# Performance work log

Measured on AMD Instinct MI355X. Metric: run time of the kernel, lower is better.

## Reference

```python
import jax, jax.numpy as jnp
import numpy as np

RES = 7          # pooler_resolution
SR = 2           # sampling_ratio
SCALES = (1.0 / 8.0, 1.0 / 16.0, 1.0 / 32.0)
IMG = 1024.0


def roi_align_one(feat, boxes, scale):
    """torchvision roi_align (aligned=True) for one image.
    feat: [C,H,W]; boxes: [N,4] (x1,y1,x2,y2) -> [N,C,RES,RES]."""
    C, H, W = feat.shape
    N = boxes.shape[0]
    b = boxes * scale - 0.5  # aligned=True offset
    x1, y1, x2, y2 = b[:, 0], b[:, 1], b[:, 2], b[:, 3]
    bh = (y2 - y1) / RES
    bw = (x2 - x1) / RES
    # sample points within each bin: y = y1 + bh*(iy + (jy+0.5)/SR)
    grid = (jnp.arange(RES, dtype=feat.dtype)[:, None]
            + (jnp.arange(SR, dtype=feat.dtype)[None, :] + 0.5) / SR).reshape(-1)  # [RES*SR]
    ys = y1[:, None] + bh[:, None] * grid[None, :]  # [N, RES*SR]
    xs = x1[:, None] + bw[:, None] * grid[None, :]

    def prep(c, size):
        m = ((c >= -1.0) & (c <= size)).astype(feat.dtype)
        cc = jnp.clip(c, 0.0, size - 1)
        lo = jnp.minimum(jnp.floor(cc).astype(jnp.int32), size - 1)
        hi = jnp.minimum(lo + 1, size - 1)
        frac = cc - lo.astype(feat.dtype)
        return lo, hi, frac, m

    y0, y1i, ly, my = prep(ys, H)
    x0, x1i, lx, mx = prep(xs, W)
    hy, hx = 1.0 - ly, 1.0 - lx
    # gather 4 corners: result [C, N, Sy, Sx]
    f00 = feat[:, y0[:, :, None], x0[:, None, :]]
    f01 = feat[:, y0[:, :, None], x1i[:, None, :]]
    f10 = feat[:, y1i[:, :, None], x0[:, None, :]]
    f11 = feat[:, y1i[:, :, None], x1i[:, None, :]]
    val = (hy[:, :, None] * (hx[:, None, :] * f00 + lx[:, None, :] * f01)
           + ly[:, :, None] * (hx[:, None, :] * f10 + lx[:, None, :] * f11))
    val = val * (my[:, :, None] * mx[:, None, :])
    pooled = val.reshape(C, N, RES, SR, RES, SR).mean(axis=(3, 5))  # avg over samples per bin
    return pooled.transpose(1, 0, 2, 3)  # [N, C, RES, RES]


def setup_inputs() -> dict:
    key = jax.random.key(0)
    ks = jax.random.split(key, 12)
    B, N, C = 4, 512, 256
    feat_p3 = jax.random.normal(ks[0], (B, C, 128, 128), jnp.float32)
    feat_p4 = jax.random.normal(ks[1], (B, C, 64, 64), jnp.float32)
    feat_p5 = jax.random.normal(ks[2], (B, C, 32, 32), jnp.float32)
    # valid boxes inside a 1024x1024 image
    cx = jax.random.uniform(ks[3], (B, N), minval=0.0, maxval=IMG)
    cy = jax.random.uniform(ks[4], (B, N), minval=0.0, maxval=IMG)
    bw = jax.random.uniform(ks[5], (B, N), minval=16.0, maxval=256.0)
    bh = jax.random.uniform(ks[6], (B, N), minval=16.0, maxval=256.0)
    x1 = jnp.clip(cx - bw / 2, 0.0, IMG - 1.0)
    y1 = jnp.clip(cy - bh / 2, 0.0, IMG - 1.0)
    x2 = jnp.clip(cx + bw / 2, x1 + 1.0, IMG)
    y2 = jnp.clip(cy + bh / 2, y1 + 1.0, IMG)
    bbox2d = jnp.stack([x1, y1, x2, y2], axis=-1)  # [B,N,4]
    anchor_id = jax.random.randint(ks[7], (B, N, 1), 0, 9, dtype=jnp.int32)
    FLAT = C * RES * RES  # 12544
    FC = 1024
    OUT = 93
    W1 = jax.random.normal(ks[8], (FC, FLAT), jnp.float32) * 0.01
    b1 = jnp.zeros((FC,), jnp.float32)
    W2 = jax.random.normal(ks[9], (FC, FC), jnp.float32) * 0.02
    b2 = jnp.zeros((FC,), jnp.float32)
    Wp = jax.random.normal(ks[10], (OUT, FC), jnp.float32) * 0.02
    bp = jnp.zeros((OUT,), jnp.float32)
    return {"feat_p3": feat_p3, "feat_p4": feat_p4, "feat_p5": feat_p5,
            "bbox2d": bbox2d, "anchor_id": anchor_id,
            "W1": W1, "b1": b1, "W2": W2, "b2": b2, "Wp": Wp, "bp": bp}


def reference(feat_p3, feat_p4, feat_p5, bbox2d, anchor_id, W1, b1, W2, b2, Wp, bp):
    B, N = bbox2d.shape[:2]
    level = anchor_id[..., 0] // 3  # [B,N] in {0,1,2}
    feats = (feat_p3, feat_p4, feat_p5)
    # pool every proposal at every level, then pick its assigned level
    pooled = None
    for l, (scale, feat) in enumerate(zip(SCALES, feats)):
        p = jax.vmap(lambda f, bx, s=scale: roi_align_one(f, bx, s))(feat, bbox2d)  # [B,N,C,R,R]
        sel = (level == l).astype(p.dtype)[..., None, None, None]
        pooled = p * sel if pooled is None else pooled + p * sel
    x = pooled.reshape(B * N, -1)  # flatten [B*N, C*R*R]
    x = jax.nn.relu(x @ W1.T + b1)
    x = jax.nn.relu(x @ W2.T + b2)
    out = x @ Wp.T + bp
    return out.reshape(B, N, -1)  # [4, 512, 93]
```

## Files before the change

### kernel.cpp

```cpp
#include <hip/hip_runtime.h>
#include <hip/hip_bf16.h>

typedef unsigned short u16;
typedef __attribute__((ext_vector_type(8))) short short8;
typedef __attribute__((ext_vector_type(4))) float f32x4;
typedef __attribute__((ext_vector_type(4))) unsigned short us4;

__device__ __forceinline__ u16 f32_bf16(float f) {
  union { float f; unsigned int u; } v; v.f = f;
  unsigned int r = v.u + 0x7fffu + ((v.u >> 16) & 1u);
  return (u16)(r >> 16);
}
__device__ __forceinline__ float bf16_f32(u16 h) {
  union { unsigned int u; float f; } v; v.u = ((unsigned int)h) << 16; return v.f;
}

__device__ __forceinline__ void load_lds16(const void* g, void* l) {
  __builtin_amdgcn_global_load_lds((const __attribute__((address_space(1))) unsigned int*)g,
                                   (__attribute__((address_space(3))) unsigned int*)l,
                                   16, 0, 0);
}

__global__ __launch_bounds__(256) void cvt_f32_bf16(
    const float* __restrict__ src, u16* __restrict__ dst, int n4) {
  int i = blockIdx.x * 256 + threadIdx.x;
  if (i >= n4) return;
  const float4 v = ((const float4*)src)[i];
  unsigned long long pk = (unsigned long long)f32_bf16(v.x)
                        | ((unsigned long long)f32_bf16(v.y) << 16)
                        | ((unsigned long long)f32_bf16(v.z) << 32)
                        | ((unsigned long long)f32_bf16(v.w) << 48);
  ((unsigned long long*)dst)[i] = pk;
}

__global__ __launch_bounds__(256) void cvt_wp(
    const float* __restrict__ src, u16* __restrict__ dst) {
  int i = blockIdx.x * 256 + threadIdx.x;
  if (i >= 24576) return;
  int e = i * 4;
  float4 v = (e < 95232) ? ((const float4*)src)[i] : float4{0.f, 0.f, 0.f, 0.f};
  unsigned long long pk = (unsigned long long)f32_bf16(v.x)
                        | ((unsigned long long)f32_bf16(v.y) << 16)
                        | ((unsigned long long)f32_bf16(v.z) << 32)
                        | ((unsigned long long)f32_bf16(v.w) << 48);
  ((unsigned long long*)dst)[i] = pk;
}

__global__ __launch_bounds__(256) void transpose_feats(
    const float* __restrict__ p3, const float* __restrict__ p4, const float* __restrict__ p5,
    u16* __restrict__ t3, u16* __restrict__ t4, u16* __restrict__ t5) {
  const int bid = blockIdx.x;
  const float* src; u16* dst; int S, tile;
  if (bid < 16384)      { src = p3; dst = t3; S = 128; tile = bid; }
  else if (bid < 20480) { src = p4; dst = t4; S = 64;  tile = bid - 16384; }
  else                  { src = p5; dst = t5; S = 32;  tile = bid - 20480; }
  const int cchunk = tile & 3;
  const int fp0 = (tile >> 2) * 16;
  const int SS = S * S;
  const int b = fp0 / SS;
  const int pimg = fp0 - b * SS;
  __shared__ __align__(16) u16 lds[16 * 72];
  const int t = threadIdx.x;
  {
    const int cl = t >> 2, xv = t & 3;
    const int c = cchunk * 64 + cl;
    const float4 v = *(const float4*)(src + (size_t)(b * 256 + c) * SS + pimg + xv * 4);
    lds[(xv * 4 + 0) * 72 + cl] = f32_bf16(v.x);
    lds[(xv * 4 + 1) * 72 + cl] = f32_bf16(v.y);
    lds[(xv * 4 + 2) * 72 + cl] = f32_bf16(v.z);
    lds[(xv * 4 + 3) * 72 + cl] = f32_bf16(v.w);
  }
  __syncthreads();
  {
    const int xl = t >> 4, cg = (t & 15) * 4;
    const us4 h = *(const us4*)&lds[xl * 72 + cg];
    *(us4*)(dst + (size_t)(fp0 + xl) * 256 + cchunk * 64 + cg) = h;
  }
}

__global__ __launch_bounds__(256) void roi_pool2(
    const u16* __restrict__ t3, const u16* __restrict__ t4, const u16* __restrict__ t5,
    const float* __restrict__ bbox, const int* __restrict__ anchor,
    u16* __restrict__ X) {
  const int m = blockIdx.x;
  const int b = m >> 9;
  const int lvl = anchor[m] / 3;
  const u16* ft; int S; float scale;
  if (lvl == 0)      { ft = t3; S = 128; scale = 0.125f;   }
  else if (lvl == 1) { ft = t4; S = 64;  scale = 0.0625f;  }
  else               { ft = t5; S = 32;  scale = 0.03125f; }
  ft += (size_t)b * S * S * 256;
  const float* bx = bbox + (size_t)m * 4;
  const float x1 = bx[0] * scale - 0.5f;
  const float y1 = bx[1] * scale - 0.5f;
  const float bw = (bx[2] * scale - 0.5f - x1) * (1.0f / 7.0f);
  const float bh = (bx[3] * scale - 0.5f - y1) * (1.0f / 7.0f);
  const float fS = (float)S;

  __shared__ __align__(16) u16 xs[12544];
  const int wave = threadIdx.x >> 6, lane = threadIdx.x & 63;
  const int cbase = lane * 4;

  for (int p = wave; p < 49; p += 4) {
    const int py = p / 7, px = p - py * 7;
    float s0 = 0.f, s1 = 0.f, s2 = 0.f, s3 = 0.f;
#pragma unroll
    for (int sy = 0; sy < 2; ++sy) {
      const float y = y1 + bh * ((float)py + (sy ? 0.75f : 0.25f));
      const float my = (y >= -1.0f && y <= fS) ? 1.0f : 0.0f;
      const float cy = fminf(fmaxf(y, 0.0f), fS - 1.0f);
      const int y0 = (int)cy;
      const float ly = cy - (float)y0;
      const float hy = 1.0f - ly;
      const int y1i = (y0 + 1 < S) ? y0 + 1 : S - 1;
#pragma unroll
      for (int sx = 0; sx < 2; ++sx) {
        const float x = x1 + bw * ((float)px + (sx ? 0.75f : 0.25f));
        const float mx = (x >= -1.0f && x <= fS) ? 1.0f : 0.0f;
        const float cx = fminf(fmaxf(x, 0.0f), fS - 1.0f);
        const int x0 = (int)cx;
        const float lx = cx - (float)x0;
        const float hx = 1.0f - lx;
        const int x1i = (x0 + 1 < S) ? x0 + 1 : S - 1;
        const us4 f00 = *(const us4*)(ft + (size_t)(y0  * S + x0 ) * 256 + cbase);
        const us4 f01 = *(const us4*)(ft + (size_t)(y0  * S + x1i) * 256 + cbase);
        const us4 f10 = *(const us4*)(ft + (size_t)(y1i * S + x0 ) * 256 + cbase);
        const us4 f11 = *(const us4*)(ft + (size_t)(y1i * S + x1i) * 256 + cbase);
        const float msk = my * mx;
        const float w00 = hy * hx * msk, w01 = hy * lx * msk;
        const float w10 = ly * hx * msk, w11 = ly * lx * msk;
        s0 += w00 * bf16_f32(f00.x) + w01 * bf16_f32(f01.x) + w10 * bf16_f32(f10.x) + w11 * bf16_f32(f11.x);
        s1 += w00 * bf16_f32(f00.y) + w01 * bf16_f32(f01.y) + w10 * bf16_f32(f10.y) + w11 * bf16_f32(f11.y);
        s2 += w00 * bf16_f32(f00.z) + w01 * bf16_f32(f01.z) + w10 * bf16_f32(f10.z) + w11 * bf16_f32(f11.z);
        s3 += w00 * bf16_f32(f00.w) + w01 * bf16_f32(f01.w) + w10 * bf16_f32(f10.w) + w11 * bf16_f32(f11.w);
      }
    }
    xs[(cbase + 0) * 49 + p] = f32_bf16(s0 * 0.25f);
    xs[(cbase + 1) * 49 + p] = f32_bf16(s1 * 0.25f);
    xs[(cbase + 2) * 49 + p] = f32_bf16(s2 * 0.25f);
    xs[(cbase + 3) * 49 + p] = f32_bf16(s3 * 0.25f);
  }
  __syncthreads();
  uint4* dst = (uint4*)(X + (size_t)m * 12544);
  const uint4* srcl = (const uint4*)xs;
  for (int i = threadIdx.x; i < 1568; i += 256) dst[i] = srcl[i];
}

template<int NT>
__global__ __launch_bounds__(512, 2)
void gemm8_bt(const u16* __restrict__ A, int lda,
              const u16* __restrict__ B, int ldb,
              u16* __restrict__ Cpart, int M, int N,
              int mb, int nb) {
  __shared__ __align__(16) char lds[131072];
  const int tid = threadIdx.x;
  const int wave = tid >> 6, lane = tid & 63;
  const int wr = wave >> 2, wc = wave & 3;

  const int G = gridDim.x;
  const int bid = blockIdx.x;
  const int swz = (bid & 7) * (G >> 3) + (bid >> 3);
  const int x = swz % mb;
  const int rest = swz / mb;
  const int y = rest % nb;
  const int z = rest / nb;
  const int m0 = x * 256, n0 = y * 256;
  const int kb0 = z * (NT * 64);

  const int sb = ((lane & 7) ^ (lane >> 3)) << 4;
  const int rowb2 = 2 * (wave * 8 + (lane >> 3)) + (sb >> 6);
  const int keloff = (sb & 63) >> 1;

  const int frow = lane & 15;
  const int rh = frow >> 1;
  const int swb = ((((frow & 1) << 6) | ((lane >> 4) << 4))) ^ (rh << 4);
  const int a_rd = wr * 8192 + rh * 128 + swb;
  const int b_rd = wc * 4096 + rh * 128 + swb;

  f32x4 acc[8][4];
#pragma unroll
  for (int i = 0; i < 8; ++i)
#pragma unroll
    for (int j = 0; j < 4; ++j)
      acc[i][j] = f32x4{0.f, 0.f, 0.f, 0.f};

  auto stageAB = [&](int tile, int ph) {
    const int dst = ((tile & 1) * 2 + ph) * 16384;
    const int kel = kb0 + tile * 64 + ph * 32 + keloff;
#pragma unroll
    for (int i = 0; i < 2; ++i) {
      const u16* srcA = A + (size_t)(m0 + i * 128 + rowb2) * lda + kel;
      load_lds16(srcA, lds + dst + i * 8192 + wave * 1024);
    }
#pragma unroll
    for (int i = 0; i < 2; ++i) {
      const u16* srcB = B + (size_t)(n0 + i * 128 + rowb2) * ldb + kel;
      load_lds16(srcB, lds + 65536 + dst + i * 8192 + wave * 1024);
    }
  };

#define GPHASE(T, PH, VW, DOSTAGE)                                              \
  {                                                                             \
    asm volatile("s_waitcnt vmcnt(" VW ")" ::: "memory");                       \
    __builtin_amdgcn_s_barrier();                                               \
    __builtin_amdgcn_sched_barrier(0);                                          \
    const int hb_ = (((T) & 1) * 2 + (PH)) * 16384;                             \
    short8 af[8], bf[4];                                                        \
    _Pragma("unroll")                                                           \
    for (int fi = 0; fi < 8; ++fi)                                              \
      af[fi] = *(const short8*)(lds + hb_ + a_rd + fi * 1024);                  \
    _Pragma("unroll")                                                           \
    for (int fj = 0; fj < 4; ++fj)                                              \
      bf[fj] = *(const short8*)(lds + 65536 + hb_ + b_rd + fj * 1024);          \
    if (DOSTAGE) stageAB((T) + 1, (PH));                                        \
    __builtin_amdgcn_s_setprio(1);                                              \
    _Pragma("unroll")                                                           \
    for (int fi = 0; fi < 8; ++fi) {                                            \
      _Pragma("unroll")                                                         \
      for (int fj = 0; fj < 4; ++fj)                                            \
        acc[fi][fj] = __builtin_amdgcn_mfma_f32_16x16x32_bf16(af[fi], bf[fj],   \
                                                              acc[fi][fj], 0, 0, 0); \
    }                                                                           \
    __builtin_amdgcn_s_setprio(0);                                              \
  }

  stageAB(0, 0);
  stageAB(0, 1);
#pragma unroll 1
  for (int t = 0; t < NT - 1; ++t) {
    GPHASE(t, 0, "4", true);
    GPHASE(t, 1, "4", true);
  }
  GPHASE(NT - 1, 0, "4", false);
  GPHASE(NT - 1, 1, "0", false);
#undef GPHASE

  u16* Cp = Cpart + (size_t)z * ((size_t)M * N);
  const int rq = (lane >> 4) * 4;
  const int cq = lane & 15;
#pragma unroll
  for (int fi = 0; fi < 8; ++fi)
#pragma unroll
    for (int fj = 0; fj < 4; ++fj) {
      const int row = m0 + wr * 128 + fi * 16 + rq;
      const int col = n0 + wc * 64 + fj * 16 + cq;
#pragma unroll
      for (int q = 0; q < 4; ++q)
        Cp[(size_t)(row + q) * N + col] = f32_bf16(acc[fi][fj][q]);
    }
}

__global__ __launch_bounds__(256) void reduce_bias7(
    const u16* __restrict__ P7, const float* __restrict__ bias,
    u16* __restrict__ out) {
  const int i4 = (blockIdx.x * 256 + threadIdx.x) * 4;
  if (i4 >= 2097152) return;
  const int nb = i4 & 1023;
  float s0 = bias[nb], s1 = bias[nb + 1], s2 = bias[nb + 2], s3 = bias[nb + 3];
#pragma unroll
  for (int j = 0; j < 7; ++j) {
    const us4 v = *(const us4*)(P7 + (size_t)j * 2097152 + i4);
    s0 += bf16_f32(v.x); s1 += bf16_f32(v.y); s2 += bf16_f32(v.z); s3 += bf16_f32(v.w);
  }
  us4 o;
  o.x = f32_bf16(fmaxf(s0, 0.f)); o.y = f32_bf16(fmaxf(s1, 0.f));
  o.z = f32_bf16(fmaxf(s2, 0.f)); o.w = f32_bf16(fmaxf(s3, 0.f));
  *(us4*)(out + i4) = o;
}

template<int BM, int BN, int WGM, int WGN>
__global__ __launch_bounds__(256)
void gemm_bt_splitk(const u16* __restrict__ A, int lda,
                    const u16* __restrict__ B, int ldb,
                    float* __restrict__ Cpart, int M, int N, int Ksplit) {
  constexpr int BK = 64;
  constexpr int WM = BM / WGM, WN = BN / WGN;
  constexpr int FM = WM / 16, FN = WN / 16;
  constexpr int AITER = BM * BK / 2048;
  constexpr int BITER = BN * BK / 2048;
  __shared__ u16 Asm_[BM * BK];
  __shared__ u16 Bsm_[BN * BK];
  const int tid = threadIdx.x;
  const int wave = tid >> 6, lane = tid & 63;
  const int wr = wave / WGN, wc = wave % WGN;
  const int m0 = blockIdx.x * BM, n0 = blockIdx.y * BN;
  const int kbase0 = blockIdx.z * Ksplit;

  f32x4 acc[FM][FN];
#pragma unroll
  for (int i = 0; i < FM; ++i)
#pragma unroll
    for (int j = 0; j < FN; ++j)
      acc[i][j] = f32x4{0.0f, 0.0f, 0.0f, 0.0f};

  const int ar = tid >> 3;
  const int acsub = (tid & 7) * 8;
  const int fr = lane & 15;
  const int kq = (lane >> 4) * 8;

  for (int kt = 0; kt < Ksplit; kt += BK) {
    const int kb = kbase0 + kt;
#pragma unroll
    for (int it = 0; it < AITER; ++it) {
      const u16* src = A + (size_t)(m0 + it * 32 + ar) * lda + kb + acsub;
      load_lds16(src, (char*)Asm_ + it * 4096 + wave * 1024);
    }
#pragma unroll
    for (int it = 0; it < BITER; ++it) {
      const u16* src = B + (size_t)(n0 + it * 32 + ar) * ldb + kb + acsub;
      load_lds16(src, (char*)Bsm_ + it * 4096 + wave * 1024);
    }
    __syncthreads();
#pragma unroll
    for (int kk = 0; kk < BK; kk += 32) {
      short8 af[FM], bfr[FN];
#pragma unroll
      for (int i = 0; i < FM; ++i)
        af[i] = *(const short8*)(Asm_ + (wr * WM + i * 16 + fr) * BK + kk + kq);
#pragma unroll
      for (int j = 0; j < FN; ++j)
        bfr[j] = *(const short8*)(Bsm_ + (wc * WN + j * 16 + fr) * BK + kk + kq);
#pragma unroll
      for (int i = 0; i < FM; ++i)
#pragma unroll
        for (int j = 0; j < FN; ++j)
          acc[i][j] = __builtin_amdgcn_mfma_f32_16x16x32_bf16(af[i], bfr[j], acc[i][j], 0, 0, 0);
    }
    __syncthreads();
  }

  float* Cp = Cpart + (size_t)blockIdx.z * ((size_t)M * N);
  const int rq = (lane >> 4) * 4;
  const int cq = lane & 15;
#pragma unroll
  for (int i = 0; i < FM; ++i)
#pragma unroll
    for (int j = 0; j < FN; ++j) {
      const int row = m0 + wr * WM + i * 16 + rq;
      const int col = n0 + wc * WN + j * 16 + cq;
      float* o = Cp + (size_t)row * N + col;
#pragma unroll
      for (int q = 0; q < 4; ++q)
        o[(size_t)q * N] = acc[i][j][q];
    }
}

template<int S, bool RELU>
__global__ __launch_bounds__(256) void reduce_bias_bf16(
    const float* __restrict__ P, const float* __restrict__ bias,
    u16* __restrict__ out, int MN, int Nmask) {
  const int i = blockIdx.x * 256 + threadIdx.x;
  if (i >= MN) return;
  float s = bias[i & Nmask];
#pragma unroll
  for (int j = 0; j < S; ++j) s += P[(size_t)j * MN + i];
  if (RELU) s = fmaxf(s, 0.0f);
  out[i] = f32_bf16(s);
}

__global__ __launch_bounds__(256) void reduce_out(
    const float* __restrict__ P, const float* __restrict__ bp,
    float* __restrict__ out) {
  const int i = blockIdx.x * 256 + threadIdx.x;
  if (i >= 2048 * 93) return;
  const int mrow = i / 93;
  const int n = i - mrow * 93;
  float s = bp[n];
#pragma unroll
  for (int j = 0; j < 8; ++j) s += P[(size_t)j * (2048 * 96) + mrow * 96 + n];
  out[i] = s;
}

extern "C" void kernel_launch(void* const* d_in, const int* in_sizes, int n_in,
                              void* d_out, int out_size, void* d_ws, size_t ws_size,
                              hipStream_t stream) {
  const float* p3   = (const float*)d_in[0];
  const float* p4   = (const float*)d_in[1];
  const float* p5   = (const float*)d_in[2];
  const float* bbox = (const float*)d_in[3];
  const int*   anc  = (const int*)d_in[4];
  const float* W1   = (const float*)d_in[5];
  const float* b1   = (const float*)d_in[6];
  const float* W2   = (const float*)d_in[7];
  const float* b2   = (const float*)d_in[8];
  const float* Wp   = (const float*)d_in[9];
  const float* bp   = (const float*)d_in[10];
  float* out = (float*)d_out;

  char* ws = (char*)d_ws;
  u16* X   = (u16*)(ws);
  u16* W1b = (u16*)(ws + 51380224);
  char* R = ws + 77070336;
  u16* t3  = (u16*)(R);
  u16* t4  = (u16*)(R + 33554432);
  u16* t5  = (u16*)(R + 41943040);
  u16* W2b = (u16*)(R);
  u16* Wpb = (u16*)(R + 2097152);
  u16* H1  = (u16*)(R + 2293760);
  u16* H2  = (u16*)(R + 6488064);
  u16*   P7 = (u16*)(R + 10682368);
  float* Pf = (float*)(R + 10682368);
  (void)ws_size; (void)in_sizes; (void)n_in; (void)out_size;

  hipLaunchKernelGGL(transpose_feats, dim3(21504), dim3(256), 0, stream, p3, p4, p5, t3, t4, t5);
  hipLaunchKernelGGL(roi_pool2, dim3(2048), dim3(256), 0, stream, t3, t4, t5, bbox, anc, X);
  hipLaunchKernelGGL(cvt_f32_bf16, dim3(12544), dim3(256), 0, stream, W1, W1b, 3211264);
  hipLaunchKernelGGL(cvt_f32_bf16, dim3(1024), dim3(256), 0, stream, W2, W2b, 262144);
  hipLaunchKernelGGL(cvt_wp, dim3(96), dim3(256), 0, stream, Wp, Wpb);
  hipLaunchKernelGGL((gemm8_bt<28>), dim3(224), dim3(512), 0, stream,
                     X, 12544, W1b, 12544, P7, 2048, 1024, 8, 4);
  hipLaunchKernelGGL(reduce_bias7, dim3(2048), dim3(256), 0, stream, P7, b1, H1);
  hipLaunchKernelGGL((gemm_bt_splitk<128,128,2,2>), dim3(16, 8, 2), dim3(256), 0, stream,
                     H1, 1024, W2b, 1024, Pf, 2048, 1024, 512);
  hipLaunchKernelGGL((reduce_bias_bf16<2,true>), dim3(8192), dim3(256), 0, stream,
                     Pf, b2, H2, 2048 * 1024, 1023);
  hipLaunchKernelGGL((gemm_bt_splitk<128,96,4,1>), dim3(16, 1, 8), dim3(256), 0, stream,
                     H2, 1024, Wpb, 1024, Pf, 2048, 96, 128);
  hipLaunchKernelGGL(reduce_out, dim3(744), dim3(256), 0, stream, Pf, bp, out);
}
```

Baseline: 193.1 us.

## Pool ROIs in packed fp16 and rebalance W1 GEMM to eight K-splits

Feature maps are now transposed into fp16 instead of bf16, and the ROI pooling kernel loads 8 channels per lane and accumulates the bilinear taps with packed fp16 vector arithmetic. Two pooled bins are processed per wave per iteration, so each gather is wider and there are fewer float conversions and FMAs. Separately, the first GEMM's split-K goes from 7 uneven partitions (224 blocks) to 8 partitions of 24 or 25 tiles (256 blocks) to fill the CUs more evenly, and the bias-reduce kernel now sums 8 partials. Accumulating in fp16 risks precision loss and overflow relative to fp32 accumulation, and the extra partial adds reduce traffic.

```diff
diff --git a/kernel.cpp b/kernel.cpp
--- a/kernel.cpp
+++ b/kernel.cpp
@@ -5,6 +5,7 @@
 typedef __attribute__((ext_vector_type(8))) short short8;
 typedef __attribute__((ext_vector_type(4))) float f32x4;
 typedef __attribute__((ext_vector_type(4))) unsigned short us4;
+typedef __attribute__((ext_vector_type(8))) _Float16 h8;
 
 __device__ __forceinline__ u16 f32_bf16(float f) {
   union { float f; unsigned int u; } v; v.f = f;
@@ -13,6 +14,14 @@
 }
 __device__ __forceinline__ float bf16_f32(u16 h) {
   union { unsigned int u; float f; } v; v.u = ((unsigned int)h) << 16; return v.f;
+}
+__device__ __forceinline__ u16 f32_f16(float f) {
+  union { _Float16 h; u16 u; } v; v.h = (_Float16)f; return v.u;
+}
+__device__ __forceinline__ h8 splat8(float f) {
+  _Float16 h = (_Float16)f;
+  h8 r = {h, h, h, h, h, h, h, h};
+  return r;
 }
 
 __device__ __forceinline__ void load_lds16(const void* g, void* l) {
@@ -65,10 +74,10 @@
     const int cl = t >> 2, xv = t & 3;
     const int c = cchunk * 64 + cl;
     const float4 v = *(const float4*)(src + (size_t)(b * 256 + c) * SS + pimg + xv * 4);
-    lds[(xv * 4 + 0) * 72 + cl] = f32_bf16(v.x);
-    lds[(xv * 4 + 1) * 72 + cl] = f32_bf16(v.y);
-    lds[(xv * 4 + 2) * 72 + cl] = f32_bf16(v.z);
-    lds[(xv * 4 + 3) * 72 + cl] = f32_bf16(v.w);
+    lds[(xv * 4 + 0) * 72 + cl] = f32_f16(v.x);
+    lds[(xv * 4 + 1) * 72 + cl] = f32_f16(v.y);
+    lds[(xv * 4 + 2) * 72 + cl] = f32_f16(v.z);
+    lds[(xv * 4 + 3) * 72 + cl] = f32_f16(v.w);
   }
   __syncthreads();
   {
@@ -78,7 +87,7 @@
   }
 }
 
-__global__ __launch_bounds__(256) void roi_pool2(
+__global__ __launch_bounds__(256) void roi_pool3(
     const u16* __restrict__ t3, const u16* __restrict__ t4, const u16* __restrict__ t5,
     const float* __restrict__ bbox, const int* __restrict__ anchor,
     u16* __restrict__ X) {
@@ -99,46 +108,48 @@
 
   __shared__ __align__(16) u16 xs[12544];
   const int wave = threadIdx.x >> 6, lane = threadIdx.x & 63;
-  const int cbase = lane * 4;
-
-  for (int p = wave; p < 49; p += 4) {
-    const int py = p / 7, px = p - py * 7;
-    float s0 = 0.f, s1 = 0.f, s2 = 0.f, s3 = 0.f;
-#pragma unroll
-    for (int sy = 0; sy < 2; ++sy) {
-      const float y = y1 + bh * ((float)py + (sy ? 0.75f : 0.25f));
-      const float my = (y >= -1.0f && y <= fS) ? 1.0f : 0.0f;
-      const float cy = fminf(fmaxf(y, 0.0f), fS - 1.0f);
-      const int y0 = (int)cy;
-      const float ly = cy - (float)y0;
-      const float hy = 1.0f - ly;
-      const int y1i = (y0 + 1 < S) ? y0 + 1 : S - 1;
-#pragma unroll
-      for (int sx = 0; sx < 2; ++sx) {
-        const float x = x1 + bw * ((float)px + (sx ? 0.75f : 0.25f));
-        const float mx = (x >= -1.0f && x <= fS) ? 1.0f : 0.0f;
-        const float cx = fminf(fmaxf(x, 0.0f), fS - 1.0f);
-        const int x0 = (int)cx;
-        const float lx = cx - (float)x0;
-        const float hx = 1.0f - lx;
-        const int x1i = (x0 + 1 < S) ? x0 + 1 : S - 1;
-        const us4 f00 = *(const us4*)(ft + (size_t)(y0  * S + x0 ) * 256 + cbase);
-        const us4 f01 = *(const us4*)(ft + (size_t)(y0  * S + x1i) * 256 + cbase);
-        const us4 f10 = *(const us4*)(ft + (size_t)(y1i * S + x0 ) * 256 + cbase);
-        const us4 f11 = *(const us4*)(ft + (size_t)(y1i * S + x1i) * 256 + cbase);
-        const float msk = my * mx;
-        const float w00 = hy * hx * msk, w01 = hy * lx * msk;
-        const float w10 = ly * hx * msk, w11 = ly * lx * msk;
-        s0 += w00 * bf16_f32(f00.x) + w01 * bf16_f32(f01.x) + w10 * bf16_f32(f10.x) + w11 * bf16_f32(f11.x);
-        s1 += w00 * bf16_f32(f00.y) + w01 * bf16_f32(f01.y) + w10 * bf16_f32(f10.y) + w11 * bf16_f32(f11.y);
-        s2 += w00 * bf16_f32(f00.z) + w01 * bf16_f32(f01.z) + w10 * bf16_f32(f10.z) + w11 * bf16_f32(f11.z);
-        s3 += w00 * bf16_f32(f00.w) + w01 * bf16_f32(f01.w) + w10 * bf16_f32(f10.w) + w11 * bf16_f32(f11.w);
+  const int l = lane & 31, h = lane >> 5;
+  const int cbase = l * 8;
+
+#pragma unroll 1
+  for (int it = 0; it < 7; ++it) {
+    const int p = it * 8 + wave * 2 + h;
+    if (p < 49) {
+      const int py = p / 7, px = p - py * 7;
+      h8 acc = splat8(0.0f);
+#pragma unroll
+      for (int sy = 0; sy < 2; ++sy) {
+        const float y = y1 + bh * ((float)py + (sy ? 0.75f : 0.25f));
+        const float my = (y >= -1.0f && y <= fS) ? 1.0f : 0.0f;
+        const float cy = fminf(fmaxf(y, 0.0f), fS - 1.0f);
+        const int y0 = (int)cy;
+        const float ly = cy - (float)y0;
+        const float hy = 1.0f - ly;
+        const int y1i = (y0 + 1 < S) ? y0 + 1 : S - 1;
+#pragma unroll
+        for (int sx = 0; sx < 2; ++sx) {
+          const float x = x1 + bw * ((float)px + (sx ? 0.75f : 0.25f));
+          const float mx = (x >= -1.0f && x <= fS) ? 1.0f : 0.0f;
+          const float cx = fminf(fmaxf(x, 0.0f), fS - 1.0f);
+          const int x0 = (int)cx;
+          const float lx = cx - (float)x0;
+          const float hx = 1.0f - lx;
+          const int x1i = (x0 + 1 < S) ? x0 + 1 : S - 1;
+          const h8 f00 = *(const h8*)(ft + (size_t)(y0  * S + x0 ) * 256 + cbase);
+          const h8 f01 = *(const h8*)(ft + (size_t)(y0  * S + x1i) * 256 + cbase);
+          const h8 f10 = *(const h8*)(ft + (size_t)(y1i * S + x0 ) * 256 + cbase);
+          const h8 f11 = *(const h8*)(ft + (size_t)(y1i * S + x1i) * 256 + cbase);
+          const float msk = my * mx;
+          acc += f00 * splat8(hy * hx * msk);
+          acc += f01 * splat8(hy * lx * msk);
+          acc += f10 * splat8(ly * hx * msk);
+          acc += f11 * splat8(ly * lx * msk);
+        }
       }
-    }
-    xs[(cbase + 0) * 49 + p] = f32_bf16(s0 * 0.25f);
-    xs[(cbase + 1) * 49 + p] = f32_bf16(s1 * 0.25f);
-    xs[(cbase + 2) * 49 + p] = f32_bf16(s2 * 0.25f);
-    xs[(cbase + 3) * 49 + p] = f32_bf16(s3 * 0.25f);
+#pragma unroll
+      for (int i = 0; i < 8; ++i)
+        xs[(cbase + i) * 49 + p] = f32_bf16((float)acc[i] * 0.25f);
+    }
   }
   __syncthreads();
   uint4* dst = (uint4*)(X + (size_t)m * 12544);
@@ -146,7 +157,6 @@
   for (int i = threadIdx.x; i < 1568; i += 256) dst[i] = srcl[i];
 }
 
-template<int NT>
 __global__ __launch_bounds__(512, 2)
 void gemm8_bt(const u16* __restrict__ A, int lda,
               const u16* __restrict__ B, int ldb,
@@ -165,7 +175,8 @@
   const int y = rest % nb;
   const int z = rest / nb;
   const int m0 = x * 256, n0 = y * 256;
-  const int kb0 = z * (NT * 64);
+  const int nt = 24 + (z < 4 ? 1 : 0);
+  const int kb0 = (z * 24 + (z < 4 ? z : 4)) * 64;
 
   const int sb = ((lane & 7) ^ (lane >> 3)) << 4;
   const int rowb2 = 2 * (wave * 8 + (lane >> 3)) + (sb >> 6);
@@ -227,12 +238,12 @@
   stageAB(0, 0);
   stageAB(0, 1);
 #pragma unroll 1
-  for (int t = 0; t < NT - 1; ++t) {
+  for (int t = 0; t < nt - 1; ++t) {
     GPHASE(t, 0, "4", true);
     GPHASE(t, 1, "4", true);
   }
-  GPHASE(NT - 1, 0, "4", false);
-  GPHASE(NT - 1, 1, "0", false);
+  GPHASE(nt - 1, 0, "4", false);
+  GPHASE(nt - 1, 1, "0", false);
 #undef GPHASE
 
   u16* Cp = Cpart + (size_t)z * ((size_t)M * N);
@@ -250,16 +261,16 @@
     }
 }
 
-__global__ __launch_bounds__(256) void reduce_bias7(
-    const u16* __restrict__ P7, const float* __restrict__ bias,
+__global__ __launch_bounds__(256) void reduce_bias8(
+    const u16* __restrict__ P8, const float* __restrict__ bias,
     u16* __restrict__ out) {
   const int i4 = (blockIdx.x * 256 + threadIdx.x) * 4;
   if (i4 >= 2097152) return;
   const int nb = i4 & 1023;
   float s0 = bias[nb], s1 = bias[nb + 1], s2 = bias[nb + 2], s3 = bias[nb + 3];
 #pragma unroll
-  for (int j = 0; j < 7; ++j) {
-    const us4 v = *(const us4*)(P7 + (size_t)j * 2097152 + i4);
+  for (int j = 0; j < 8; ++j) {
+    const us4 v = *(const us4*)(P8 + (size_t)j * 2097152 + i4);
     s0 += bf16_f32(v.x); s1 += bf16_f32(v.y); s2 += bf16_f32(v.z); s3 += bf16_f32(v.w);
   }
   us4 o;
@@ -398,18 +409,18 @@
   u16* Wpb = (u16*)(R + 2097152);
   u16* H1  = (u16*)(R + 2293760);
   u16* H2  = (u16*)(R + 6488064);
-  u16*   P7 = (u16*)(R + 10682368);
+  u16*   P8 = (u16*)(R + 10682368);
   float* Pf = (float*)(R + 10682368);
   (void)ws_size; (void)in_sizes; (void)n_in; (void)out_size;
 
   hipLaunchKernelGGL(transpose_feats, dim3(21504), dim3(256), 0, stream, p3, p4, p5, t3, t4, t5);
-  hipLaunchKernelGGL(roi_pool2, dim3(2048), dim3(256), 0, stream, t3, t4, t5, bbox, anc, X);
+  hipLaunchKernelGGL(roi_pool3, dim3(2048), dim3(256), 0, stream, t3, t4, t5, bbox, anc, X);
   hipLaunchKernelGGL(cvt_f32_bf16, dim3(12544), dim3(256), 0, stream, W1, W1b, 3211264);
   hipLaunchKernelGGL(cvt_f32_bf16, dim3(1024), dim3(256), 0, stream, W2, W2b, 262144);
   hipLaunchKernelGGL(cvt_wp, dim3(96), dim3(256), 0, stream, Wp, Wpb);
-  hipLaunchKernelGGL((gemm8_bt<28>), dim3(224), dim3(512), 0, stream,
-                     X, 12544, W1b, 12544, P7, 2048, 1024, 8, 4);
-  hipLaunchKernelGGL(reduce_bias7, dim3(2048), dim3(256), 0, stream, P7, b1, H1);
+  hipLaunchKernelGGL(gemm8_bt, dim3(256), dim3(512), 0, stream,
+                     X, 12544, W1b, 12544, P8, 2048, 1024, 8, 4);
+  hipLaunchKernelGGL(reduce_bias8, dim3(2048), dim3(256), 0, stream, P8, b1, H1);
   hipLaunchKernelGGL((gemm_bt_splitk<128,128,2,2>), dim3(16, 8, 2), dim3(256), 0, stream,
                      H1, 1024, W2b, 1024, Pf, 2048, 1024, 512);
   hipLaunchKernelGGL((reduce_bias_bf16<2,true>), dim3(8192), dim3(256), 0, stream,
```

Result: faster. 175.6 us (-9.0%).
